# Kernel tuning notes

Hardware: AMD Instinct MI355X
Metric: run time of the kernel (lower is better)

The kernel has to match this reference:

```python
import jax, jax.numpy as jnp
import numpy as np

L = 500_000      # total nodes across all graphs
D = 256          # d_model
G = 4096         # number of graphs
EPS_SOFTMAX = 1e-7
EPS_LN = 1e-5


def setup_inputs() -> dict:
    key = jax.random.key(0)
    ks = jax.random.split(key, 6)
    f_node = jax.random.normal(ks[0], (L, D), dtype=jnp.float32)
    key_W = jax.random.normal(ks[1], (D, D), dtype=jnp.float32) * 0.02
    key_b = jnp.zeros((D,), dtype=jnp.float32)
    value_W = jax.random.normal(ks[2], (D, D), dtype=jnp.float32) * 0.02
    value_b = jnp.zeros((D,), dtype=jnp.float32)
    gamma = jnp.ones((D,), dtype=jnp.float32)
    beta = jnp.zeros((D,), dtype=jnp.float32)
    graph_id = jax.random.randint(ks[3], (L,), 0, G, dtype=jnp.int32)
    return {
        "f_node": f_node,
        "key_W": key_W,
        "key_b": key_b,
        "value_W": value_W,
        "value_b": value_b,
        "gamma": gamma,
        "beta": beta,
        "graph_id": graph_id,
        "num_graphs": G,
    }


def reference(f_node, key_W, key_b, value_W, value_b, gamma, beta, graph_id, num_graphs):
    # attn scores: Linear(key)  -> [L, D]
    attn = f_node @ key_W.T + key_b
    # scatter_softmax over nodes within each graph (per feature column)
    seg_max = jax.ops.segment_max(attn, graph_id, num_segments=num_graphs)  # [G, D]
    ex = jnp.exp(attn - seg_max[graph_id])                                   # [L, D]
    seg_sum = jax.ops.segment_sum(ex, graph_id, num_segments=num_graphs)    # [G, D]
    attn = ex / (seg_sum[graph_id] + EPS_SOFTMAX)
    # weighted aggregation of value projection -> [G, D]
    val = f_node @ value_W.T + value_b
    f_graph = jax.ops.segment_sum(val * attn, graph_id, num_segments=num_graphs)
    # LayerNorm (dropout is identity in eval mode)
    mu = jnp.mean(f_graph, axis=-1, keepdims=True)
    var = jnp.mean(jnp.square(f_graph - mu), axis=-1, keepdims=True)
    return (f_graph - mu) * jax.lax.rsqrt(var + EPS_LN) * gamma + beta
```

## Files before the change

### kernel.cpp

```cpp
#include <hip/hip_runtime.h>

typedef short short8 __attribute__((ext_vector_type(8)));
typedef float floatx4 __attribute__((ext_vector_type(4)));

#define GPB 8

__device__ __forceinline__ unsigned short f2bf(float x) {
  union { float f; unsigned int u; } c; c.f = x;
  return (unsigned short)((c.u + 0x7FFFu + ((c.u >> 16) & 1u)) >> 16);
}

__device__ __forceinline__ unsigned cvtpk(float lo, float hi) {
  unsigned r;
  asm("v_cvt_pk_bf16_f32 %0, %1, %2" : "=v"(r) : "v"(lo), "v"(hi));
  return r;
}

__device__ __forceinline__ void gld16(const void* g, void* l) {
  __builtin_amdgcn_global_load_lds((const __attribute__((address_space(1))) void*)g,
                                   (__attribute__((address_space(3))) void*)l, 16, 0, 0);
}
__device__ __forceinline__ void gld4(const void* g, void* l) {
  __builtin_amdgcn_global_load_lds((const __attribute__((address_space(1))) void*)g,
                                   (__attribute__((address_space(3))) void*)l, 4, 0, 0);
}

__global__ void k_hist(const int* __restrict__ gid, int L, int* __restrict__ counts) {
  int i = blockIdx.x * blockDim.x + threadIdx.x;
  if (i < L) atomicAdd(&counts[gid[i]], 1);
}

__global__ void k_scan(const int* __restrict__ counts, int* __restrict__ offsets,
                       int* __restrict__ cursor, int G) {
  __shared__ int sc[1024];
  int t = threadIdx.x;
  int items = (G + 1023) >> 10;
  int base = t * items;
  int s = 0;
  for (int i = 0; i < items; ++i) { int idx = base + i; if (idx < G) s += counts[idx]; }
  sc[t] = s;
  __syncthreads();
  for (int off = 1; off < 1024; off <<= 1) {
    int v = (t >= off) ? sc[t - off] : 0;
    __syncthreads();
    if (t >= off) sc[t] += v;
    __syncthreads();
  }
  int run = (t == 0) ? 0 : sc[t - 1];
  for (int i = 0; i < items; ++i) {
    int idx = base + i;
    if (idx < G) { offsets[idx] = run; cursor[idx] = run; run += counts[idx]; }
  }
  if (t == 1023) offsets[G] = sc[1023];
}

__global__ void k_scatter(const int* __restrict__ gid, int L, int* __restrict__ cursor,
                          int* __restrict__ order) {
  int i = blockIdx.x * blockDim.x + threadIdx.x;
  if (i < L) {
    int g = gid[i];
    int pos = atomicAdd(&cursor[g], 1);
    order[pos] = i;
  }
}

__global__ void k_prepw(const float* __restrict__ keyW, const float* __restrict__ valW,
                        unsigned short* __restrict__ W2) {
  int j2 = blockIdx.x;
  int k = threadIdx.x;
  int wv = j2 >> 6, half = (j2 >> 5) & 1, c = j2 & 31;
  int d = (wv << 5) + c;
  const float* src = half ? valW : keyW;
  W2[j2 * 256 + k] = f2bf(src[d * 256 + k]);
}

__launch_bounds__(512, 2)
__global__ void k_fused(const float* __restrict__ fnode,
                        const unsigned short* __restrict__ W2,
                        const float* __restrict__ key_b, const float* __restrict__ value_b,
                        const float* __restrict__ gamma, const float* __restrict__ beta,
                        const int* __restrict__ order, const int* __restrict__ offsets,
                        float* __restrict__ out, int L, int Gtot) {
  __shared__ __align__(16) float f32stage[64 * 256];
  __shared__ __align__(16) unsigned short bfA[2][64 * 256];
  __shared__ float fg[GPB][256];
  __shared__ int ord_ring[2][64];
  __shared__ int eb[GPB + 1];
  __shared__ float redS[4], redS2[4];

  const int t = threadIdx.x;
  const int lane = t & 63;
  const int w = t >> 6;
  const int lcol = lane & 15;
  const int lrow = lane >> 4;
  const int g0 = blockIdx.x * GPB;

  if (t <= GPB) eb[t] = offsets[min(g0 + t, Gtot)];
  __syncthreads();
  const int rbase = eb[0];
  const int nrows = eb[GPB] - rbase;
  const int nc = max(1, (nrows + 63) >> 6);

  float kb[2], vb[2];
#pragma unroll
  for (int nj = 0; nj < 2; ++nj) {
    int d = (w << 5) + (nj << 4) + lcol;
    kb[nj] = key_b[d];
    vb[nj] = value_b[d];
  }

  const unsigned short* Wn[4];
#pragma unroll
  for (int nj = 0; nj < 4; ++nj)
    Wn[nj] = W2 + ((size_t)((w << 6) + ((nj >> 1) << 5) + ((nj & 1) << 4) + lcol)) * 256 +
             lrow * 8;

  short8 bp[4][4];
#pragma unroll
  for (int nj = 0; nj < 4; ++nj)
#pragma unroll
    for (int kk = 0; kk < 4; ++kk)
      bp[nj][kk] = *reinterpret_cast<const short8*>(Wn[nj] + kk * 32);

  float den[2] = {0.f, 0.f};
  float num[2] = {0.f, 0.f};

  auto stage_ord = [&](int c) {
    if (w == 0) {
      int pos = rbase + (c << 6) + lane;
      if (pos >= L) pos = L - 1;
      gld4(order + pos, &ord_ring[c & 1][0]);
    }
  };
  auto stage_rows = [&](int c) {
#pragma unroll
    for (int it = 0; it < 8; ++it) {
      const int idx = ord_ring[c & 1][(w << 3) + it];
      const char* gsrc =
          (const char*)fnode + ((size_t)idx << 10) + ((lane << 4) ^ (it << 4));
      gld16(gsrc, (char*)f32stage + (((w << 3) + it) << 10));
    }
  };

  int curg = 0;
  int ecur = eb[1] - rbase;
  int flushed = 0;

  stage_ord(0);
  asm volatile("s_waitcnt vmcnt(0)" ::: "memory");
  __syncthreads();
  stage_rows(0);
  if (nc > 1) stage_ord(1);

  for (int c = 0; c < nc; ++c) {
    const int m0 = c << 6;

    asm volatile("s_waitcnt vmcnt(0)" ::: "memory");
    __syncthreads();

    {
      const int r = t >> 3, q = t & 7, x7 = r & 7;
      const char* fsrow = (const char*)f32stage + (r << 10);
      char* bfrow = (char*)&bfA[c & 1][0] + (r << 9);
#pragma unroll
      for (int i = 0; i < 4; ++i) {
        const int S0 = 8 * q + 2 * i;
        const floatx4 a = *(const floatx4*)(fsrow + ((S0 ^ x7) << 4));
        const floatx4 b2 = *(const floatx4*)(fsrow + (((S0 + 1) ^ x7) << 4));
        uint4 o;
        o.x = cvtpk(a[0], a[1]);
        o.y = cvtpk(a[2], a[3]);
        o.z = cvtpk(b2[0], b2[1]);
        o.w = cvtpk(b2[2], b2[3]);
        *(uint4*)(bfrow + (((4 * q + i) ^ x7) << 4)) = o;
      }
    }
    __syncthreads();

    if (c + 1 < nc) {
      stage_rows(c + 1);
      if (c + 2 < nc) stage_ord(c + 2);
    }

    const char* bfb = (const char*)&bfA[c & 1][0];
    floatx4 acc[4][4];
#pragma unroll
    for (int mi = 0; mi < 4; ++mi)
#pragma unroll
      for (int nj = 0; nj < 4; ++nj)
        acc[mi][nj] = (floatx4){0.f, 0.f, 0.f, 0.f};

    __builtin_amdgcn_s_setprio(1);
#pragma unroll
    for (int kk = 0; kk < 8; ++kk) {
      short8 afr[4];
#pragma unroll
      for (int mi = 0; mi < 4; ++mi) {
        const int row = mi * 16 + lcol;
        afr[mi] = *reinterpret_cast<const short8*>(
            bfb + (row << 9) + ((((kk << 2) + lrow) ^ (row & 7)) << 4));
      }
#pragma unroll
      for (int nj = 0; nj < 4; ++nj) {
        const short8 bfr = (kk < 4)
                               ? bp[nj][kk]
                               : *reinterpret_cast<const short8*>(Wn[nj] + (kk << 5));
#pragma unroll
        for (int mi = 0; mi < 4; ++mi)
          acc[mi][nj] =
              __builtin_amdgcn_mfma_f32_16x16x32_bf16(afr[mi], bfr, acc[mi][nj], 0, 0, 0);
      }
    }
    __builtin_amdgcn_s_setprio(0);

    {
      int lo = 0;
      while (true) {
        const int hi = min(ecur - m0, 64);
#pragma unroll
        for (int mi = 0; mi < 4; ++mi)
#pragma unroll
          for (int qq = 0; qq < 4; ++qq) {
            const int r = mi * 16 + lrow * 4 + qq;
            const bool in = (r >= lo) && (r < hi);
#pragma unroll
            for (int nj = 0; nj < 2; ++nj) {
              const float a = acc[mi][nj][qq] + kb[nj];
              const float v = acc[mi][nj + 2][qq] + vb[nj];
              const float e_ = in ? __expf(a) : 0.f;
              den[nj] += e_;
              num[nj] += v * e_;
            }
          }
        if (ecur <= m0 + 64) {
#pragma unroll
          for (int nj = 0; nj < 2; ++nj) {
            float ds = den[nj], ns = num[nj];
            ds += __shfl_xor(ds, 16, 64);
            ds += __shfl_xor(ds, 32, 64);
            ns += __shfl_xor(ns, 16, 64);
            ns += __shfl_xor(ns, 32, 64);
            if (lrow == 0)
              fg[curg & (GPB - 1)][(w << 5) + (nj << 4) + lcol] = ns / (ds + 1e-7f);
            den[nj] = 0.f;
            num[nj] = 0.f;
          }
          ++curg;
          lo = hi;
          ecur = (curg < GPB) ? (eb[curg + 1] - rbase) : 0x7fffffff;
        } else
          break;
        if (curg >= GPB) break;
      }
    }

    if (curg > flushed) {
      __syncthreads();
      for (int j = flushed; j < curg; ++j) {
        float x = 0.f;
        if (t < 256) x = fg[j & (GPB - 1)][t];
        float s = x, s2 = x * x;
#pragma unroll
        for (int o = 32; o > 0; o >>= 1) {
          s += __shfl_xor(s, o, 64);
          s2 += __shfl_xor(s2, o, 64);
        }
        if (t < 256 && lane == 0) { redS[w] = s; redS2[w] = s2; }
        __syncthreads();
        if (t < 256 && (g0 + j) < Gtot) {
          const float ts = redS[0] + redS[1] + redS[2] + redS[3];
          const float ts2 = redS2[0] + redS2[1] + redS2[2] + redS2[3];
          const float mu = ts * (1.f / 256.f);
          const float var = ts2 * (1.f / 256.f) - mu * mu;
          const float inv = rsqrtf(var + 1e-5f);
          out[(size_t)(g0 + j) * 256 + t] = (x - mu) * inv * gamma[t] + beta[t];
        }
        __syncthreads();
      }
      flushed = curg;
    }
  }
}

extern "C" void kernel_launch(void* const* d_in, const int* in_sizes, int n_in,
                              void* d_out, int out_size, void* d_ws, size_t ws_size,
                              hipStream_t stream) {
  const float* f_node   = (const float*)d_in[0];
  const float* key_W    = (const float*)d_in[1];
  const float* key_b    = (const float*)d_in[2];
  const float* value_W  = (const float*)d_in[3];
  const float* value_b  = (const float*)d_in[4];
  const float* gamma    = (const float*)d_in[5];
  const float* beta     = (const float*)d_in[6];
  const int*   graph_id = (const int*)d_in[7];
  const int L = in_sizes[0] / 256;
  const int G = out_size / 256;

  char* ws = (char*)d_ws;
  size_t off = 0;
  int* order = (int*)(ws + off); off += (size_t)L * 4;
  off = (off + 255) & ~(size_t)255;
  int* counts = (int*)(ws + off); off += (size_t)G * 4;
  int* offsets = (int*)(ws + off); off += (size_t)(G + 1) * 4;
  int* cursor = (int*)(ws + off); off += (size_t)G * 4;
  off = (off + 255) & ~(size_t)255;
  unsigned short* W2 = (unsigned short*)(ws + off); off += 512 * 256 * 2;

  hipMemsetAsync(counts, 0, (size_t)G * 4, stream);
  k_hist<<<(L + 255) / 256, 256, 0, stream>>>(graph_id, L, counts);
  k_scan<<<1, 1024, 0, stream>>>(counts, offsets, cursor, G);
  k_scatter<<<(L + 255) / 256, 256, 0, stream>>>(graph_id, L, cursor, order);
  k_prepw<<<512, 256, 0, stream>>>(key_W, value_W, W2);
  const int nblk = (G + GPB - 1) / GPB;
  k_fused<<<nblk, 512, 0, stream>>>(f_node, W2, key_b, value_b, gamma, beta, order,
                                    offsets, (float*)d_out, L, G);
}
```

Measured before the change: 376.2 us.

## Prefetch rows into registers and convert to bf16 directly, halving graphs per block

Replaces the async global-to-LDS fp32 staging with double-buffered bf16 tiles by register prefetch. The next chunk's rows are loaded into registers before the MFMA loop, then converted and written into a single bf16 LDS tile after the epilogue. It also preloads the block's order indices into LDS up front, halves graphs per block to 4 (more blocks, less LDS), and keeps more of W in registers (6 of 8 k-slices). This cuts LDS footprint and the separate conversion pass, at the cost of more register pressure and an extra barrier per chunk.

```diff
diff --git a/kernel.cpp b/kernel.cpp
--- a/kernel.cpp
+++ b/kernel.cpp
@@ -3,7 +3,8 @@
 typedef short short8 __attribute__((ext_vector_type(8)));
 typedef float floatx4 __attribute__((ext_vector_type(4)));
 
-#define GPB 8
+#define GPB 4
+#define ORD_CAP 768
 
 __device__ __forceinline__ unsigned short f2bf(float x) {
   union { float f; unsigned int u; } c; c.f = x;
@@ -14,15 +15,6 @@
   unsigned r;
   asm("v_cvt_pk_bf16_f32 %0, %1, %2" : "=v"(r) : "v"(lo), "v"(hi));
   return r;
-}
-
-__device__ __forceinline__ void gld16(const void* g, void* l) {
-  __builtin_amdgcn_global_load_lds((const __attribute__((address_space(1))) void*)g,
-                                   (__attribute__((address_space(3))) void*)l, 16, 0, 0);
-}
-__device__ __forceinline__ void gld4(const void* g, void* l) {
-  __builtin_amdgcn_global_load_lds((const __attribute__((address_space(1))) void*)g,
-                                   (__attribute__((address_space(3))) void*)l, 4, 0, 0);
 }
 
 __global__ void k_hist(const int* __restrict__ gid, int L, int* __restrict__ counts) {
@@ -81,10 +73,9 @@
                         const float* __restrict__ gamma, const float* __restrict__ beta,
                         const int* __restrict__ order, const int* __restrict__ offsets,
                         float* __restrict__ out, int L, int Gtot) {
-  __shared__ __align__(16) float f32stage[64 * 256];
-  __shared__ __align__(16) unsigned short bfA[2][64 * 256];
+  __shared__ __align__(16) unsigned short As[64 * 256];
+  __shared__ int ord_s[ORD_CAP];
   __shared__ float fg[GPB][256];
-  __shared__ int ord_ring[2][64];
   __shared__ int eb[GPB + 1];
   __shared__ float redS[4], redS2[4];
 
@@ -98,8 +89,10 @@
   if (t <= GPB) eb[t] = offsets[min(g0 + t, Gtot)];
   __syncthreads();
   const int rbase = eb[0];
-  const int nrows = eb[GPB] - rbase;
-  const int nc = max(1, (nrows + 63) >> 6);
+  const int span = eb[GPB] - rbase;
+  const int nc = max(1, (span + 63) >> 6);
+
+  for (int i = t; i < ORD_CAP; i += 512) ord_s[i] = order[min(rbase + i, L - 1)];
 
   float kb[2], vb[2];
 #pragma unroll
@@ -108,81 +101,57 @@
     kb[nj] = key_b[d];
     vb[nj] = value_b[d];
   }
-
   const unsigned short* Wn[4];
 #pragma unroll
   for (int nj = 0; nj < 4; ++nj)
     Wn[nj] = W2 + ((size_t)((w << 6) + ((nj >> 1) << 5) + ((nj & 1) << 4) + lcol)) * 256 +
              lrow * 8;
-
-  short8 bp[4][4];
+  short8 bp[4][6];
 #pragma unroll
   for (int nj = 0; nj < 4; ++nj)
 #pragma unroll
-    for (int kk = 0; kk < 4; ++kk)
-      bp[nj][kk] = *reinterpret_cast<const short8*>(Wn[nj] + kk * 32);
-
+    for (int kk = 0; kk < 6; ++kk)
+      bp[nj][kk] = *reinterpret_cast<const short8*>(Wn[nj] + (kk << 5));
+
+  __syncthreads();
+
+  float4 fl[8];
+  auto issue = [&](int c) {
+#pragma unroll
+    for (int it = 0; it < 8; ++it) {
+      int gi = (c << 6) + (w << 3) + it;
+      gi = min(gi, span - 1);
+      if (gi < 0) gi = 0;
+      const int idx = (gi < ORD_CAP) ? ord_s[gi] : order[rbase + gi];
+      fl[it] = *reinterpret_cast<const float4*>(fnode + (size_t)idx * 256 + (lane << 2));
+    }
+  };
+  auto stwr = [&]() {
+#pragma unroll
+    for (int it = 0; it < 8; ++it) {
+      const int r = (w << 3) + it;
+      uint2 v;
+      v.x = cvtpk(fl[it].x, fl[it].y);
+      v.y = cvtpk(fl[it].z, fl[it].w);
+      char* p = (char*)As + (r << 9) + ((((lane >> 1) ^ it) << 4) | ((lane & 1) << 3));
+      *reinterpret_cast<uint2*>(p) = v;
+    }
+  };
+
+  issue(0);
+  __builtin_amdgcn_sched_barrier(0);
+  stwr();
+  __syncthreads();
+
+  int curg = 0, flushed = 0;
+  int ecur = eb[1] - rbase;
   float den[2] = {0.f, 0.f};
   float num[2] = {0.f, 0.f};
 
-  auto stage_ord = [&](int c) {
-    if (w == 0) {
-      int pos = rbase + (c << 6) + lane;
-      if (pos >= L) pos = L - 1;
-      gld4(order + pos, &ord_ring[c & 1][0]);
-    }
-  };
-  auto stage_rows = [&](int c) {
-#pragma unroll
-    for (int it = 0; it < 8; ++it) {
-      const int idx = ord_ring[c & 1][(w << 3) + it];
-      const char* gsrc =
-          (const char*)fnode + ((size_t)idx << 10) + ((lane << 4) ^ (it << 4));
-      gld16(gsrc, (char*)f32stage + (((w << 3) + it) << 10));
-    }
-  };
-
-  int curg = 0;
-  int ecur = eb[1] - rbase;
-  int flushed = 0;
-
-  stage_ord(0);
-  asm volatile("s_waitcnt vmcnt(0)" ::: "memory");
-  __syncthreads();
-  stage_rows(0);
-  if (nc > 1) stage_ord(1);
-
   for (int c = 0; c < nc; ++c) {
-    const int m0 = c << 6;
-
-    asm volatile("s_waitcnt vmcnt(0)" ::: "memory");
-    __syncthreads();
-
-    {
-      const int r = t >> 3, q = t & 7, x7 = r & 7;
-      const char* fsrow = (const char*)f32stage + (r << 10);
-      char* bfrow = (char*)&bfA[c & 1][0] + (r << 9);
-#pragma unroll
-      for (int i = 0; i < 4; ++i) {
-        const int S0 = 8 * q + 2 * i;
-        const floatx4 a = *(const floatx4*)(fsrow + ((S0 ^ x7) << 4));
-        const floatx4 b2 = *(const floatx4*)(fsrow + (((S0 + 1) ^ x7) << 4));
-        uint4 o;
-        o.x = cvtpk(a[0], a[1]);
-        o.y = cvtpk(a[2], a[3]);
-        o.z = cvtpk(b2[0], b2[1]);
-        o.w = cvtpk(b2[2], b2[3]);
-        *(uint4*)(bfrow + (((4 * q + i) ^ x7) << 4)) = o;
-      }
-    }
-    __syncthreads();
-
-    if (c + 1 < nc) {
-      stage_rows(c + 1);
-      if (c + 2 < nc) stage_ord(c + 2);
-    }
-
-    const char* bfb = (const char*)&bfA[c & 1][0];
+    issue(c + 1 < nc ? c + 1 : c);
+    __builtin_amdgcn_sched_barrier(0);
+
     floatx4 acc[4][4];
 #pragma unroll
     for (int mi = 0; mi < 4; ++mi)
@@ -198,11 +167,11 @@
       for (int mi = 0; mi < 4; ++mi) {
         const int row = mi * 16 + lcol;
         afr[mi] = *reinterpret_cast<const short8*>(
-            bfb + (row << 9) + ((((kk << 2) + lrow) ^ (row & 7)) << 4));
+            (const char*)As + (row << 9) + ((((kk << 2) | lrow) ^ (row & 7)) << 4));
       }
 #pragma unroll
       for (int nj = 0; nj < 4; ++nj) {
-        const short8 bfr = (kk < 4)
+        const short8 bfr = (kk < 6)
                                ? bp[nj][kk]
                                : *reinterpret_cast<const short8*>(Wn[nj] + (kk << 5));
 #pragma unroll
@@ -213,6 +182,7 @@
     }
     __builtin_amdgcn_s_setprio(0);
 
+    const int m0 = c << 6;
     {
       int lo = 0;
       while (true) {
@@ -279,6 +249,12 @@
       }
       flushed = curg;
     }
+
+    __syncthreads();
+    if (c + 1 < nc) {
+      stwr();
+      __syncthreads();
+    }
   }
 }
 
```

Measured after the change: 707.4 us. 88.1% more time.
